# Kernel optimization log

Measured on AMD Instinct MI355X. Metric: run time of the kernel, lower is better.

Reference implementation:

```python
import jax, jax.numpy as jnp
import numpy as np
from jax import lax

K = 5  # up_kernel_size

def nearest_up2(x):
    # PyTorch F.interpolate(scale_factor=2) default mode='nearest': out[i]=in[i//2]
    return jnp.repeat(jnp.repeat(x, 2, axis=2), 2, axis=3)

def conv1x1(x, W, b=None):
    # x: [B,C,H,W], W: [O,C]
    y = jnp.einsum('bchw,oc->bohw', x, W)
    if b is not None:
        y = y + b[None, :, None, None]
    return y

def depthwise3x3(x, W, b):
    # x: [B,25,H,W], W: [25,1,3,3] (OIHW with groups=25)
    y = lax.conv_general_dilated(x, W, window_strides=(1, 1), padding='SAME',
                                 feature_group_count=x.shape[1],
                                 dimension_numbers=('NCHW', 'OIHW', 'NCHW'))
    return y + b[None, :, None, None]

def carafe(de, kernels):
    # de: [B,C,H,W]; kernels: [B,K*K,2H,2W], softmax-normalized over channel dim
    B, C, H, Wd = de.shape
    r = K // 2
    de_p = jnp.pad(de, ((0, 0), (0, 0), (r, r), (r, r)))
    # patches[b,k,c,h,w] = de neighborhood, k = dy*K+dx  -> [B,25,C,H,W]
    patches = jnp.stack([de_p[:, :, dy:dy + H, dx:dx + Wd]
                         for dy in range(K) for dx in range(K)], axis=1)
    # kernels[b,k,2h+s,2w+t] -> [B,25,H,2,W,2]; source pixel is (i//2, j//2)
    kr = kernels.reshape(B, K * K, H, 2, Wd, 2)
    out = jnp.einsum('bkchw,bkhswt->bchswt', patches, kr)
    return out.reshape(B, C, 2 * H, 2 * Wd)

def setup_inputs() -> dict:
    key = jax.random.key(0)
    ks = jax.random.split(key, 8)
    B, C, H, W = 4, 256, 64, 64
    en = jax.random.normal(ks[0], (B, C, 2 * H, 2 * W), dtype=jnp.float32)
    de = jax.random.normal(ks[1], (B, C, H, W), dtype=jnp.float32)
    s = 1.0 / np.sqrt(C)
    W_gate = jax.random.uniform(ks[2], (1, C), jnp.float32, -s, s)
    b_gate = jnp.zeros((1,), jnp.float32)
    W_ce = jax.random.uniform(ks[3], (K * K, C), jnp.float32, -s, s)
    b_ce = jnp.zeros((K * K,), jnp.float32)
    W_cd = jax.random.uniform(ks[4], (K * K, C), jnp.float32, -s, s)
    W_dw = jax.random.uniform(ks[5], (K * K, 1, 3, 3), jnp.float32, -0.33, 0.33)
    b_dw = jnp.zeros((K * K,), jnp.float32)
    return {'en': en, 'de': de, 'W_gate': W_gate, 'b_gate': b_gate,
            'W_ce': W_ce, 'b_ce': b_ce, 'W_cd': W_cd, 'W_dw': W_dw, 'b_dw': b_dw}

def reference(en, de, W_gate, b_gate, W_ce, b_ce, W_cd, W_dw, b_dw):
    # gate generator
    gate = jax.nn.sigmoid(nearest_up2(conv1x1(de, W_gate, b_gate)))  # [B,1,2H,2W]
    # kernel generator (SemiShiftDepthWise)
    enc = conv1x1(en, W_ce, b_ce)      # [B,25,2H,2W]
    dec = conv1x1(de, W_cd)            # [B,25,H,W]
    raw = depthwise3x3(enc, W_dw, b_dw) + nearest_up2(depthwise3x3(dec, W_dw, b_dw))
    kernels = jax.nn.softmax(raw, axis=1)
    return gate * en + (1.0 - gate) * carafe(de, kernels)
```

## Files before the change

### kernel.cpp

```cpp
#include <hip/hip_runtime.h>


typedef unsigned short u16;
typedef unsigned int u32;

#define NB 4
#define NC 256
#define NH 64
#define NW 64
#define NH2 128
#define NW2 128

#define OFF_WG   0
#define OFF_BG   256
#define OFF_WCE  272
#define OFF_BCE  6672
#define OFF_WCD  6704
#define OFF_WDW  13104
#define OFF_BDW  13330
#define OFF_FLAG 13356

#define OFF_GATE 16384
#define OFF_KB   32768
#define OFF_ENC  851968
#define OFF_DEC  2490368
#define OFF_DET  851968
#define OFF_P1   851968
#define FULL_NEED_BYTES 12877824ull

#define NGATE 16384
#define NDEC  20480
#define NENC  122880
#define NKBF  532480

__device__ __forceinline__ float bf2f(u16 u){ return __uint_as_float(((u32)u) << 16); }
__device__ __forceinline__ u16 f2bf(float f){
  u32 x = __float_as_uint(f);
  return (u16)((x + 0x7fffu + ((x >> 16) & 1u)) >> 16);
}
__device__ __forceinline__ float ldin(const void* p, int i, bool f32){
  return f32 ? ((const float*)p)[i] : bf2f(((const u16*)p)[i]);
}

__global__ __launch_bounds__(256) void k_detect(const void* de_raw, float* ws){
  __shared__ int cnt;
  if (threadIdx.x == 0) cnt = 0;
  __syncthreads();
  int c = 0;
#pragma unroll
  for (int s = 0; s < 2; s++) {
    int i = (threadIdx.x + s * 256) * 2;
    u16 u = ((const u16*)de_raw)[i];
    int e = (u >> 7) & 0xff;
    if (e >= 0x70 && e <= 0x82) c++;
  }
  atomicAdd(&cnt, c);
  __syncthreads();
  if (threadIdx.x == 0) ws[OFF_FLAG] = (cnt < 256) ? 1.0f : 0.0f;
}

__global__ __launch_bounds__(256) void k_prep(const void* Wg, const void* bg,
    const void* Wce, const void* bce, const void* Wcd, const void* Wdw, const void* bdw,
    float* ws){
  bool f = ws[OFF_FLAG] != 0.f;
  int i = threadIdx.x + blockIdx.x * 256;
  if (i < 6400) {
    ws[OFF_WCE + i] = ldin(Wce, i, f);
    ws[OFF_WCD + i] = ldin(Wcd, i, f);
    if (i < 256) ws[OFF_WG + i] = ldin(Wg, i, f);
    if (i < 1)   ws[OFF_BG + i] = ldin(bg, i, f);
    if (i < 25)  ws[OFF_BCE + i] = ldin(bce, i, f);
    if (i < 225) ws[OFF_WDW + i] = ldin(Wdw, i, f);
    if (i < 25)  ws[OFF_BDW + i] = ldin(bdw, i, f);
  }
}


__global__ __launch_bounds__(256) void o1a_dec_gate(const void* de, float* ws){
  __shared__ float red[4][26][64];
  bool f = ws[OFF_FLAG] != 0.f;
  int b = blockIdx.x >> 7;
  int rem = blockIdx.x & 127;
  int h = rem >> 1;
  int chunk = rem & 1;
  int g = threadIdx.x >> 6;
  int w = threadIdx.x & 63;
  int c0 = __builtin_amdgcn_readfirstlane(chunk * 128 + g * 32);
  float acc[26];
#pragma unroll
  for (int o = 0; o < 26; o++) acc[o] = 0.f;
  int idx = ((b * NC + c0) * NH + h) * NW + w;
  for (int ci = 0; ci < 32; ci += 8) {
    float v0 = ldin(de, idx,            f);
    float v1 = ldin(de, idx + 1 * 4096, f);
    float v2 = ldin(de, idx + 2 * 4096, f);
    float v3 = ldin(de, idx + 3 * 4096, f);
    float v4 = ldin(de, idx + 4 * 4096, f);
    float v5 = ldin(de, idx + 5 * 4096, f);
    float v6 = ldin(de, idx + 6 * 4096, f);
    float v7 = ldin(de, idx + 7 * 4096, f);
    idx += 8 * 4096;
    int c = c0 + ci;
    acc[25] += ws[OFF_WG + c] * v0 + ws[OFF_WG + c + 1] * v1
             + ws[OFF_WG + c + 2] * v2 + ws[OFF_WG + c + 3] * v3
             + ws[OFF_WG + c + 4] * v4 + ws[OFF_WG + c + 5] * v5
             + ws[OFF_WG + c + 6] * v6 + ws[OFF_WG + c + 7] * v7;
#pragma unroll
    for (int k = 0; k < 25; k++) {
      const float* wk = ws + OFF_WCD + k * 256 + c;
      acc[k] += wk[0] * v0 + wk[1] * v1 + wk[2] * v2 + wk[3] * v3
              + wk[4] * v4 + wk[5] * v5 + wk[6] * v6 + wk[7] * v7;
    }
  }
#pragma unroll
  for (int o = 0; o < 26; o++) red[g][o][w] = acc[o];
  __syncthreads();
  for (int item = threadIdx.x; item < 26 * 64; item += 256) {
    int o = item >> 6; int ww = item & 63;
    float s = red[0][o][ww] + red[1][o][ww] + red[2][o][ww] + red[3][o][ww];
    ws[OFF_P1 + (((chunk * NB + b) * 26 + o) << 12) + (h << 6) + ww] = s;
  }
}

__global__ __launch_bounds__(256) void o1b_reduce(float* ws){
  int i = blockIdx.x * 256 + threadIdx.x;
  int b = i / (26 * 4096);
  int r = i - b * 26 * 4096;
  int o = r >> 12;
  int pix = r & 4095;
  float s = ws[OFF_P1 + (((0 * NB + b) * 26 + o) << 12) + pix]
          + ws[OFF_P1 + (((1 * NB + b) * 26 + o) << 12) + pix];
  if (o < 25)
    ws[OFF_DEC + ((b * 25 + o) << 12) + pix] = s;
  else {
    float z = s + ws[OFF_BG];
    ws[OFF_GATE + (b << 12) + pix] = 1.f / (1.f + __expf(-z));
  }
}

__global__ __launch_bounds__(256) void o2_det(const void* de, float* ws){
  bool f = ws[OFF_FLAG] != 0.f;
  u16* det = (u16*)(ws + OFF_DET);
  int b = blockIdx.x / 68;
  int p = blockIdx.x % 68;
  int c = threadIdx.x;
  int h = p - 2;
  bool hv = (h >= 0 && h < NH);
  int sbase = ((b * NC + c) * NH + (hv ? h : 0)) * NW;
  u16* dst = det + ((b * 68 + p) * 68) * NC + c;
  for (int q = 0; q < 68; q++) {
    int w = q - 2;
    float v = (hv && w >= 0 && w < NW) ? ldin(de, sbase + w, f) : 0.f;
    dst[q * NC] = f2bf(v);
  }
}

__global__ __launch_bounds__(256) void o3_enc(const void* en, float* ws){
  __shared__ float red[4][25][64];
  bool f = ws[OFF_FLAG] != 0.f;
  int b = blockIdx.x >> 8;
  int rem = blockIdx.x & 255;
  int y = rem >> 1;
  int xs = (rem & 1) << 6;
  int g = threadIdx.x >> 6;
  int xl = threadIdx.x & 63;
  int c0 = __builtin_amdgcn_readfirstlane(g * 64);
  float acc[25];
#pragma unroll
  for (int k = 0; k < 25; k++) acc[k] = 0.f;
  int idx = ((b * NC + c0) * NH2 + y) * NW2 + xs + xl;
  for (int ci = 0; ci < 64; ci += 8) {
    float v0 = ldin(en, idx,             f);
    float v1 = ldin(en, idx + 1 * 16384, f);
    float v2 = ldin(en, idx + 2 * 16384, f);
    float v3 = ldin(en, idx + 3 * 16384, f);
    float v4 = ldin(en, idx + 4 * 16384, f);
    float v5 = ldin(en, idx + 5 * 16384, f);
    float v6 = ldin(en, idx + 6 * 16384, f);
    float v7 = ldin(en, idx + 7 * 16384, f);
    idx += 8 * 16384;
    int c = c0 + ci;
#pragma unroll
    for (int k = 0; k < 25; k++) {
      const float* wk = ws + OFF_WCE + k * 256 + c;
      acc[k] += wk[0] * v0 + wk[1] * v1 + wk[2] * v2 + wk[3] * v3
              + wk[4] * v4 + wk[5] * v5 + wk[6] * v6 + wk[7] * v7;
    }
  }
#pragma unroll
  for (int k = 0; k < 25; k++) red[g][k][xl] = acc[k];
  __syncthreads();
  for (int item = threadIdx.x; item < 25 * 64; item += 256) {
    int k = item >> 6; int xx = item & 63;
    float s = red[0][k][xx] + red[1][k][xx] + red[2][k][xx] + red[3][k][xx]
            + ws[OFF_BCE + k];
    ws[OFF_ENC + ((b * 25 + k) * NH2 + y) * NW2 + xs + xx] = s;
  }
}

__global__ __launch_bounds__(256) void o4_kernels(float* ws){
  __shared__ float red[25][64];
  int b = blockIdx.x >> 8;
  int rem = blockIdx.x & 255;
  int y = rem >> 1;
  int xs = (rem & 1) << 6;
  int tg = __builtin_amdgcn_readfirstlane(threadIdx.x >> 6);
  int xl = threadIdx.x & 63;
  int x = xs + xl;
  int h = y >> 1, w = x >> 1;
  const float* enc = ws + OFF_ENC + (b * 25) * NH2 * NW2;
  const float* dec = ws + OFF_DEC + (b * 25) * NH * NW;

  for (int k = tg; k < 25; k += 4) {
    float s = 2.f * ws[OFF_BDW + k];
#pragma unroll
    for (int u = 0; u < 3; u++) {
      int yy = y + u - 1, hh = h + u - 1;
      bool yok = (yy >= 0 && yy < NH2);
      bool hok = (hh >= 0 && hh < NH);
#pragma unroll
      for (int v = 0; v < 3; v++) {
        int xx = x + v - 1, w2 = w + v - 1;
        float wd = ws[OFF_WDW + k * 9 + u * 3 + v];
        if (yok && xx >= 0 && xx < NW2)
          s += enc[(k * NH2 + yy) * NW2 + xx] * wd;
        if (hok && w2 >= 0 && w2 < NW)
          s += dec[(k * NH + hh) * NW + w2] * wd;
      }
    }
    red[k][xl] = s;
  }
  __syncthreads();

  if (threadIdx.x < 64) {
    int t = threadIdx.x;
    int xp = xs + t;
    float m = -1e30f;
#pragma unroll
    for (int k = 0; k < 25; k++) m = fmaxf(m, red[k][t]);
    float sum = 0.f;
#pragma unroll
    for (int k = 0; k < 25; k++) {
      float e = __expf(red[k][t] - m);
      red[k][t] = e;
      sum += e;
    }
    float inv = 1.f / sum;
    int st = ((y & 1) << 1) + (xp & 1);
    int wp = xp >> 1;
    u16* kbu = (u16*)(ws + OFF_KB);
    u16* dst = kbu + ((b * NH + h) * NW + wp) * 100 + st;
#pragma unroll
    for (int k = 0; k < 25; k++) dst[k * 4] = f2bf(red[k][t] * inv);
  }
}

__global__ __launch_bounds__(256) void o5_final(const void* en, float* ws, float* out){
  __shared__ u16 stag[2][32][260];
  bool f = ws[OFF_FLAG] != 0.f;
  const u16* det = (const u16*)(ws + OFF_DET);
  const u16* kbu = (const u16*)(ws + OFF_KB);
  const float* gate = ws + OFF_GATE;

  int b = blockIdx.x >> 8;
  int rem = blockIdx.x & 255;
  int h = rem >> 2;
  int w0b = (rem & 3) * 16;
  int wave = threadIdx.x >> 6;
  int lane = threadIdx.x & 63;
  int c4 = lane * 4;

  for (int i = 0; i < 4; i++) {
    int wu = __builtin_amdgcn_readfirstlane(w0b + wave * 4 + i);
    const u16* kp = kbu + ((b * NH + h) * NW + wu) * 100;
    float acc[4][4];
#pragma unroll
    for (int st = 0; st < 4; st++)
#pragma unroll
      for (int j = 0; j < 4; j++) acc[st][j] = 0.f;

#pragma unroll
    for (int dy = 0; dy < 5; dy++) {
      const u16* dp = det + (((b * 68 + h + dy) * 68 + wu) * NC) + c4;
#pragma unroll
      for (int dx = 0; dx < 5; dx++) {
        ushort4 uv = *(const ushort4*)(dp + dx * NC);
        float v0 = bf2f(uv.x), v1 = bf2f(uv.y), v2 = bf2f(uv.z), v3 = bf2f(uv.w);
        const u32* kpu = (const u32*)(kp + (dy * 5 + dx) * 4);
        u32 k01 = kpu[0], k23 = kpu[1];
        float k0 = bf2f((u16)(k01 & 0xffffu));
        float k1 = bf2f((u16)(k01 >> 16));
        float k2 = bf2f((u16)(k23 & 0xffffu));
        float k3 = bf2f((u16)(k23 >> 16));
        acc[0][0] += k0 * v0; acc[0][1] += k0 * v1; acc[0][2] += k0 * v2; acc[0][3] += k0 * v3;
        acc[1][0] += k1 * v0; acc[1][1] += k1 * v1; acc[1][2] += k1 * v2; acc[1][3] += k1 * v3;
        acc[2][0] += k2 * v0; acc[2][1] += k2 * v1; acc[2][2] += k2 * v2; acc[2][3] += k2 * v3;
        acc[3][0] += k3 * v0; acc[3][1] += k3 * v1; acc[3][2] += k3 * v2; acc[3][3] += k3 * v3;
      }
    }
    int xl = (wave * 4 + i) * 2;
#pragma unroll
    for (int s = 0; s < 2; s++)
#pragma unroll
      for (int t = 0; t < 2; t++) {
        int st = s * 2 + t;
        ushort4 pv;
        pv.x = f2bf(acc[st][0]); pv.y = f2bf(acc[st][1]);
        pv.z = f2bf(acc[st][2]); pv.w = f2bf(acc[st][3]);
        *(ushort4*)&stag[s][xl + t][c4] = pv;
      }
  }
  __syncthreads();

  int xp = threadIdx.x & 31;
  int cb = (threadIdx.x >> 5) * 2;
  int x = w0b * 2 + xp;
  int wpix = w0b + (xp >> 1);
  float g = gate[(b * NH + h) * NW + wpix];
  float gi = 1.f - g;
#pragma unroll
  for (int pass = 0; pass < 16; pass++) {
    int c = cb + pass * 16;
#pragma unroll
    for (int s = 0; s < 2; s++) {
      int y = 2 * h + s;
      u32 rr = *(const u32*)&stag[s][xp][c];
      float cr0 = bf2f((u16)(rr & 0xffffu));
      float cr1 = bf2f((u16)(rr >> 16));
      int eidx = ((b * NC + c) * NH2 + y) * NW2 + x;
      float e0 = ldin(en, eidx, f);
      float e1 = ldin(en, eidx + NH2 * NW2, f);
      out[eidx] = g * e0 + gi * cr0;
      out[eidx + NH2 * NW2] = g * e1 + gi * cr1;
    }
  }
}


__global__ __launch_bounds__(256) void kA_gate(const void* de, float* ws, int b){
  bool f = ws[OFF_FLAG] != 0.f;
  int idx = blockIdx.x * 256 + threadIdx.x;
  int h = idx >> 6, w = idx & 63;
  float s = ws[OFF_BG];
  for (int c = 0; c < NC; c++)
    s += ldin(de, ((b * NC + c) * NH + h) * NW + w, f) * ws[OFF_WG + c];
  ws[NGATE + idx] = 1.f / (1.f + __expf(-s));
}

__global__ __launch_bounds__(256) void kB_dec(const void* de, float* ws, int b){
  bool f = ws[OFF_FLAG] != 0.f;
  int idx = blockIdx.x * 256 + threadIdx.x;
  int h = idx >> 6, w = idx & 63;
  float acc[25];
#pragma unroll
  for (int k = 0; k < 25; k++) acc[k] = 0.f;
  for (int c = 0; c < NC; c++) {
    float v = ldin(de, ((b * NC + c) * NH + h) * NW + w, f);
#pragma unroll
    for (int k = 0; k < 25; k++) acc[k] += v * ws[OFF_WCD + k * 256 + c];
  }
#pragma unroll
  for (int k = 0; k < 25; k++)
    ws[NDEC + (k * NH + h) * NW + w] = acc[k];
}

__global__ __launch_bounds__(256) void kC_enc(const void* en, float* ws, int b){
  bool f = ws[OFF_FLAG] != 0.f;
  int idx = blockIdx.x * 256 + threadIdx.x;
  int y = idx >> 7, x = idx & 127;
  float acc[25];
#pragma unroll
  for (int k = 0; k < 25; k++) acc[k] = 0.f;
  for (int c = 0; c < NC; c++) {
    float v = ldin(en, ((b * NC + c) * NH2 + y) * NW2 + x, f);
#pragma unroll
    for (int k = 0; k < 25; k++) acc[k] += v * ws[OFF_WCE + k * 256 + c];
  }
#pragma unroll
  for (int k = 0; k < 25; k++)
    ws[NENC + (k * NH2 + y) * NW2 + x] = acc[k] + ws[OFF_BCE + k];
}

__global__ __launch_bounds__(256) void kD_kern(float* ws){
  int idx = blockIdx.x * 256 + threadIdx.x;
  int y = idx >> 7, x = idx & 127;
  int h = y >> 1, w = x >> 1;
  float raw[25];
#pragma unroll
  for (int k = 0; k < 25; k++) {
    float s = 2.f * ws[OFF_BDW + k];
#pragma unroll
    for (int u = 0; u < 3; u++) {
      int yy = y + u - 1, hh = h + u - 1;
#pragma unroll
      for (int v = 0; v < 3; v++) {
        int xx = x + v - 1, ww = w + v - 1;
        float wd = ws[OFF_WDW + k * 9 + u * 3 + v];
        if (yy >= 0 && yy < NH2 && xx >= 0 && xx < NW2)
          s += ws[NENC + (k * NH2 + yy) * NW2 + xx] * wd;
        if (hh >= 0 && hh < NH && ww >= 0 && ww < NW)
          s += ws[NDEC + (k * NH + hh) * NW + ww] * wd;
      }
    }
    raw[k] = s;
  }
  float m = raw[0];
#pragma unroll
  for (int k = 1; k < 25; k++) m = fmaxf(m, raw[k]);
  float sum = 0.f;
#pragma unroll
  for (int k = 0; k < 25; k++) { raw[k] = __expf(raw[k] - m); sum += raw[k]; }
  float inv = 1.f / sum;
  float* dst = ws + NKBF + idx * 25;
#pragma unroll
  for (int k = 0; k < 25; k++) dst[k] = raw[k] * inv;
}

__global__ __launch_bounds__(256) void kE_out(const void* en, const void* de,
    const float* ws, float* out, int b){
  bool f = ws[OFF_FLAG] != 0.f;
  int idx = blockIdx.x * 256 + threadIdx.x;
  int c = idx >> 14;
  int y = (idx >> 7) & 127;
  int x = idx & 127;
  int h = y >> 1, w = x >> 1;
  const float* kb = ws + NKBF + (y * NW2 + x) * 25;
  float acc = 0.f;
#pragma unroll
  for (int dy = 0; dy < 5; dy++) {
    int hh = h + dy - 2;
    if (hh < 0 || hh >= NH) continue;
#pragma unroll
    for (int dx = 0; dx < 5; dx++) {
      int ww = w + dx - 2;
      if (ww < 0 || ww >= NW) continue;
      acc += ldin(de, ((b * NC + c) * NH + hh) * NW + ww, f) * kb[dy * 5 + dx];
    }
  }
  float g = ws[NGATE + h * NW + w];
  float e = ldin(en, ((b * NC + c) * NH2 + y) * NW2 + x, f);
  out[((b * NC + c) * NH2 + y) * NW2 + x] = g * e + (1.f - g) * acc;
}

static const void* find_by_size(void* const* d_in, const int* in_sizes, int n_in,
                                int want, int skip, const void* fb){
  int seen = 0;
  for (int i = 0; i < n_in; i++)
    if (in_sizes[i] == want) {
      if (seen == skip) return d_in[i];
      seen++;
    }
  return fb;
}

extern "C" void kernel_launch(void* const* d_in, const int* in_sizes, int n_in,
                              void* d_out, int out_size, void* d_ws, size_t ws_size,
                              hipStream_t stream) {
  (void)out_size;
  const void* en  = find_by_size(d_in, in_sizes, n_in, 4*256*128*128, 0, d_in[0]);
  const void* de  = find_by_size(d_in, in_sizes, n_in, 4*256*64*64,   0, d_in[1]);
  const void* Wg  = find_by_size(d_in, in_sizes, n_in, 256,           0, d_in[2]);
  const void* bg  = find_by_size(d_in, in_sizes, n_in, 1,             0, d_in[3]);
  const void* Wce = find_by_size(d_in, in_sizes, n_in, 6400,          0, d_in[4]);
  const void* bce = find_by_size(d_in, in_sizes, n_in, 25,            0, d_in[5]);
  const void* Wcd = find_by_size(d_in, in_sizes, n_in, 6400,          1, d_in[6]);
  const void* Wdw = find_by_size(d_in, in_sizes, n_in, 225,           0, d_in[7]);
  const void* bdw = find_by_size(d_in, in_sizes, n_in, 25,            1, d_in[8]);
  float* ws = (float*)d_ws;
  float* out = (float*)d_out;

  hipLaunchKernelGGL(k_detect, dim3(1), dim3(256), 0, stream, de, ws);
  hipLaunchKernelGGL(k_prep, dim3(25), dim3(256), 0, stream,
                     Wg, bg, Wce, bce, Wcd, Wdw, bdw, ws);

  if (ws_size >= FULL_NEED_BYTES) {
    hipLaunchKernelGGL(o1a_dec_gate, dim3(NB * NH * 2),  dim3(256), 0, stream, de, ws);
    hipLaunchKernelGGL(o1b_reduce,   dim3(1664),         dim3(256), 0, stream, ws);
    hipLaunchKernelGGL(o3_enc,       dim3(NB * NH2 * 2), dim3(256), 0, stream, en, ws);
    hipLaunchKernelGGL(o4_kernels,   dim3(NB * NH2 * 2), dim3(256), 0, stream, ws);
    hipLaunchKernelGGL(o2_det,       dim3(NB * 68),      dim3(256), 0, stream, de, ws);
    hipLaunchKernelGGL(o5_final,     dim3(NB * NH * 4),  dim3(256), 0, stream, en, ws, out);
  } else {
    for (int b = 0; b < NB; b++) {
      hipLaunchKernelGGL(kA_gate, dim3(16),    dim3(256), 0, stream, de, ws, b);
      hipLaunchKernelGGL(kB_dec,  dim3(16),    dim3(256), 0, stream, de, ws, b);
      hipLaunchKernelGGL(kC_enc,  dim3(64),    dim3(256), 0, stream, en, ws, b);
      hipLaunchKernelGGL(kD_kern, dim3(64),    dim3(256), 0, stream, ws);
      hipLaunchKernelGGL(kE_out,  dim3(16384), dim3(256), 0, stream, en, de, ws, out, b);
    }
  }
}
```

Measured before the change: 269.0 us.

## Split final CARAFE pass by output row parity, transpose det through shared memory

After: 249.3 us. 7.3% less time.

```diff
diff --git a/kernel.cpp b/kernel.cpp
--- a/kernel.cpp
+++ b/kernel.cpp
@@ -139,19 +139,27 @@
 }
 
 __global__ __launch_bounds__(256) void o2_det(const void* de, float* ws){
+  __shared__ float tile[64][65];
   bool f = ws[OFF_FLAG] != 0.f;
   u16* det = (u16*)(ws + OFF_DET);
-  int b = blockIdx.x / 68;
-  int p = blockIdx.x % 68;
-  int c = threadIdx.x;
+  int b = blockIdx.x / 272;
+  int r = blockIdx.x % 272;
+  int p = r >> 2;
+  int c0 = (r & 3) << 6;
   int h = p - 2;
   bool hv = (h >= 0 && h < NH);
-  int sbase = ((b * NC + c) * NH + (hv ? h : 0)) * NW;
-  u16* dst = det + ((b * 68 + p) * 68) * NC + c;
-  for (int q = 0; q < 68; q++) {
+  for (int item = threadIdx.x; item < 64 * 64; item += 256) {
+    int cl = item >> 6, w = item & 63;
+    float v = hv ? ldin(de, ((b * NC + c0 + cl) * NH + h) * NW + w, f) : 0.f;
+    tile[w][cl] = v;
+  }
+  __syncthreads();
+  u16* dst = det + ((b * 68 + p) * 68) * NC + c0;
+  for (int item = threadIdx.x; item < 68 * 64; item += 256) {
+    int q = item >> 6, cl = item & 63;
     int w = q - 2;
-    float v = (hv && w >= 0 && w < NW) ? ldin(de, sbase + w, f) : 0.f;
-    dst[q * NC] = f2bf(v);
+    float v = (w >= 0 && w < NW) ? tile[w][cl] : 0.f;
+    dst[q * NC + cl] = f2bf(v);
   }
 }
 
@@ -256,14 +264,19 @@
 }
 
 __global__ __launch_bounds__(256) void o5_final(const void* en, float* ws, float* out){
-  __shared__ u16 stag[2][32][260];
+  __shared__ u16 stag[32][260];
   bool f = ws[OFF_FLAG] != 0.f;
   const u16* det = (const u16*)(ws + OFF_DET);
   const u16* kbu = (const u16*)(ws + OFF_KB);
   const float* gate = ws + OFF_GATE;
 
-  int b = blockIdx.x >> 8;
-  int rem = blockIdx.x & 255;
+  int bi = blockIdx.x;
+  int xcd = bi & 7;
+  int slot = bi >> 3;
+  int s = slot & 1;
+  int pid = ((slot >> 1) << 3) | xcd;
+  int b = pid >> 8;
+  int rem = pid & 255;
   int h = rem >> 2;
   int w0b = (rem & 3) * 16;
   int wave = threadIdx.x >> 6;
@@ -272,12 +285,12 @@
 
   for (int i = 0; i < 4; i++) {
     int wu = __builtin_amdgcn_readfirstlane(w0b + wave * 4 + i);
-    const u16* kp = kbu + ((b * NH + h) * NW + wu) * 100;
-    float acc[4][4];
-#pragma unroll
-    for (int st = 0; st < 4; st++)
-#pragma unroll
-      for (int j = 0; j < 4; j++) acc[st][j] = 0.f;
+    const u16* kp = kbu + ((b * NH + h) * NW + wu) * 100 + s * 2;
+    float acc[2][4];
+#pragma unroll
+    for (int t = 0; t < 2; t++)
+#pragma unroll
+      for (int j = 0; j < 4; j++) acc[t][j] = 0.f;
 
 #pragma unroll
     for (int dy = 0; dy < 5; dy++) {
@@ -286,29 +299,21 @@
       for (int dx = 0; dx < 5; dx++) {
         ushort4 uv = *(const ushort4*)(dp + dx * NC);
         float v0 = bf2f(uv.x), v1 = bf2f(uv.y), v2 = bf2f(uv.z), v3 = bf2f(uv.w);
-        const u32* kpu = (const u32*)(kp + (dy * 5 + dx) * 4);
-        u32 k01 = kpu[0], k23 = kpu[1];
-        float k0 = bf2f((u16)(k01 & 0xffffu));
-        float k1 = bf2f((u16)(k01 >> 16));
-        float k2 = bf2f((u16)(k23 & 0xffffu));
-        float k3 = bf2f((u16)(k23 >> 16));
+        u32 kk = *(const u32*)(kp + (dy * 5 + dx) * 4);
+        float k0 = bf2f((u16)(kk & 0xffffu));
+        float k1 = bf2f((u16)(kk >> 16));
         acc[0][0] += k0 * v0; acc[0][1] += k0 * v1; acc[0][2] += k0 * v2; acc[0][3] += k0 * v3;
         acc[1][0] += k1 * v0; acc[1][1] += k1 * v1; acc[1][2] += k1 * v2; acc[1][3] += k1 * v3;
-        acc[2][0] += k2 * v0; acc[2][1] += k2 * v1; acc[2][2] += k2 * v2; acc[2][3] += k2 * v3;
-        acc[3][0] += k3 * v0; acc[3][1] += k3 * v1; acc[3][2] += k3 * v2; acc[3][3] += k3 * v3;
       }
     }
     int xl = (wave * 4 + i) * 2;
 #pragma unroll
-    for (int s = 0; s < 2; s++)
-#pragma unroll
-      for (int t = 0; t < 2; t++) {
-        int st = s * 2 + t;
-        ushort4 pv;
-        pv.x = f2bf(acc[st][0]); pv.y = f2bf(acc[st][1]);
-        pv.z = f2bf(acc[st][2]); pv.w = f2bf(acc[st][3]);
-        *(ushort4*)&stag[s][xl + t][c4] = pv;
-      }
+    for (int t = 0; t < 2; t++) {
+      ushort4 pv;
+      pv.x = f2bf(acc[t][0]); pv.y = f2bf(acc[t][1]);
+      pv.z = f2bf(acc[t][2]); pv.w = f2bf(acc[t][3]);
+      *(ushort4*)&stag[xl + t][c4] = pv;
+    }
   }
   __syncthreads();
 
@@ -316,23 +321,20 @@
   int cb = (threadIdx.x >> 5) * 2;
   int x = w0b * 2 + xp;
   int wpix = w0b + (xp >> 1);
+  int y = 2 * h + s;
   float g = gate[(b * NH + h) * NW + wpix];
   float gi = 1.f - g;
 #pragma unroll
   for (int pass = 0; pass < 16; pass++) {
     int c = cb + pass * 16;
-#pragma unroll
-    for (int s = 0; s < 2; s++) {
-      int y = 2 * h + s;
-      u32 rr = *(const u32*)&stag[s][xp][c];
-      float cr0 = bf2f((u16)(rr & 0xffffu));
-      float cr1 = bf2f((u16)(rr >> 16));
-      int eidx = ((b * NC + c) * NH2 + y) * NW2 + x;
-      float e0 = ldin(en, eidx, f);
-      float e1 = ldin(en, eidx + NH2 * NW2, f);
-      out[eidx] = g * e0 + gi * cr0;
-      out[eidx + NH2 * NW2] = g * e1 + gi * cr1;
-    }
+    u32 rr = *(const u32*)&stag[xp][c];
+    float cr0 = bf2f((u16)(rr & 0xffffu));
+    float cr1 = bf2f((u16)(rr >> 16));
+    int eidx = ((b * NC + c) * NH2 + y) * NW2 + x;
+    float e0 = ldin(en, eidx, f);
+    float e1 = ldin(en, eidx + NH2 * NW2, f);
+    __builtin_nontemporal_store(g * e0 + gi * cr0, &out[eidx]);
+    __builtin_nontemporal_store(g * e1 + gi * cr1, &out[eidx + NH2 * NW2]);
   }
 }
 
@@ -474,12 +476,12 @@
                      Wg, bg, Wce, bce, Wcd, Wdw, bdw, ws);
 
   if (ws_size >= FULL_NEED_BYTES) {
-    hipLaunchKernelGGL(o1a_dec_gate, dim3(NB * NH * 2),  dim3(256), 0, stream, de, ws);
-    hipLaunchKernelGGL(o1b_reduce,   dim3(1664),         dim3(256), 0, stream, ws);
-    hipLaunchKernelGGL(o3_enc,       dim3(NB * NH2 * 2), dim3(256), 0, stream, en, ws);
-    hipLaunchKernelGGL(o4_kernels,   dim3(NB * NH2 * 2), dim3(256), 0, stream, ws);
-    hipLaunchKernelGGL(o2_det,       dim3(NB * 68),      dim3(256), 0, stream, de, ws);
-    hipLaunchKernelGGL(o5_final,     dim3(NB * NH * 4),  dim3(256), 0, stream, en, ws, out);
+    hipLaunchKernelGGL(o1a_dec_gate, dim3(NB * NH * 2),     dim3(256), 0, stream, de, ws);
+    hipLaunchKernelGGL(o1b_reduce,   dim3(1664),            dim3(256), 0, stream, ws);
+    hipLaunchKernelGGL(o3_enc,       dim3(NB * NH2 * 2),    dim3(256), 0, stream, en, ws);
+    hipLaunchKernelGGL(o4_kernels,   dim3(NB * NH2 * 2),    dim3(256), 0, stream, ws);
+    hipLaunchKernelGGL(o2_det,       dim3(NB * 68 * 4),     dim3(256), 0, stream, de, ws);
+    hipLaunchKernelGGL(o5_final,     dim3(NB * NH * 4 * 2), dim3(256), 0, stream, en, ws, out);
   } else {
     for (int b = 0; b < NB; b++) {
       hipLaunchKernelGGL(kA_gate, dim3(16),    dim3(256), 0, stream, de, ws, b);
```
